# Optimization experiments

Hardware: AMD Instinct MI355X
Metric: run time of the kernel (lower is better)

The kernel has to match this reference:

```python
import jax, jax.numpy as jnp
import numpy as np

N, E, G = 30000, 480000, 64
IN, MID, HEADS, OUT = 256, (64, 64, 128), 8, 13


def _tconv(x, src, dst, ea, qw, qb, kw, kb, vw, vb, ew, sw, sb, heads, n):
    # PyG TransformerConv (concat=True, root_weight=True, beta=False), eval mode
    d = qw.shape[1] // heads
    q = (x @ qw + qb)[dst].reshape(-1, heads, d)   # [E,H,d] query at target
    k = (x @ kw + kb)[src].reshape(-1, heads, d)   # [E,H,d] key at source
    v = (x @ vw + vb)[src].reshape(-1, heads, d)   # [E,H,d] value at source
    e = (ea @ ew).reshape(-1, heads, d)            # [E,H,d] edge embedding (no bias)
    k = k + e
    a = (q * k).sum(-1) / jnp.sqrt(jnp.asarray(d, x.dtype))   # [E,H]
    amax = jax.ops.segment_max(a, dst, num_segments=n)        # segment softmax over in-edges
    ex = jnp.exp(a - amax[dst])
    den = jax.ops.segment_sum(ex, dst, num_segments=n)
    alpha = ex / den[dst]
    out = jax.ops.segment_sum((v + e) * alpha[..., None], dst, num_segments=n)
    out = out.reshape(n, heads * d)
    return out + x @ sw + sb                        # root/skip connection


def _mk(key, shape):
    return jax.random.normal(key, shape, dtype=jnp.float32) * 0.05


def setup_inputs() -> dict:
    key = jax.random.key(0)
    ks = iter(jax.random.split(key, 40))
    inp = {
        "x": jax.random.normal(next(ks), (N, IN), dtype=jnp.float32),
        "edge_index": jax.random.randint(next(ks), (2, E), 0, N, dtype=jnp.int64),
        "edge_attr": jax.random.normal(next(ks), (E, 1), dtype=jnp.float32),
        "batch": jnp.sort(jax.random.randint(next(ks), (N,), 0, G, dtype=jnp.int64)),
    }
    # conv1: in=256 -> heads=8, d=64 (out 512)
    o1 = HEADS * MID[0]
    inp.update(q1w=_mk(next(ks), (IN, o1)), q1b=_mk(next(ks), (o1,)),
               k1w=_mk(next(ks), (IN, o1)), k1b=_mk(next(ks), (o1,)),
               v1w=_mk(next(ks), (IN, o1)), v1b=_mk(next(ks), (o1,)),
               e1w=_mk(next(ks), (1, o1)),
               s1w=_mk(next(ks), (IN, o1)), s1b=_mk(next(ks), (o1,)))
    # conv2: in=512 -> heads=4, d=64 (out 256)
    h2, i2 = HEADS // 2, o1
    o2 = h2 * MID[1]
    inp.update(q2w=_mk(next(ks), (i2, o2)), q2b=_mk(next(ks), (o2,)),
               k2w=_mk(next(ks), (i2, o2)), k2b=_mk(next(ks), (o2,)),
               v2w=_mk(next(ks), (i2, o2)), v2b=_mk(next(ks), (o2,)),
               e2w=_mk(next(ks), (1, o2)),
               s2w=_mk(next(ks), (i2, o2)), s2b=_mk(next(ks), (o2,)))
    # conv3: in=256 -> heads=1, d=128
    i3, o3 = o2, MID[2]
    inp.update(q3w=_mk(next(ks), (i3, o3)), q3b=_mk(next(ks), (o3,)),
               k3w=_mk(next(ks), (i3, o3)), k3b=_mk(next(ks), (o3,)),
               v3w=_mk(next(ks), (i3, o3)), v3b=_mk(next(ks), (o3,)),
               e3w=_mk(next(ks), (1, o3)),
               s3w=_mk(next(ks), (i3, o3)), s3b=_mk(next(ks), (o3,)))
    inp.update(lw=_mk(next(ks), (MID[2], OUT)), lb=_mk(next(ks), (OUT,)))
    return inp


def reference(x, edge_index, edge_attr, batch,
              q1w, q1b, k1w, k1b, v1w, v1b, e1w, s1w, s1b,
              q2w, q2b, k2w, k2b, v2w, v2b, e2w, s2w, s2b,
              q3w, q3b, k3w, k3b, v3w, v3b, e3w, s3w, s3b,
              lw, lb):
    src, dst = edge_index[0], edge_index[1]
    h = _tconv(x, src, dst, edge_attr, q1w, q1b, k1w, k1b, v1w, v1b, e1w, s1w, s1b, HEADS, N)
    h = jax.nn.relu(h)
    h = _tconv(h, src, dst, edge_attr, q2w, q2b, k2w, k2b, v2w, v2b, e2w, s2w, s2b, HEADS // 2, N)
    h = jax.nn.relu(h)
    h = _tconv(h, src, dst, edge_attr, q3w, q3b, k3w, k3b, v3w, v3b, e3w, s3w, s3b, 1, N)
    # global mean pool over graphs
    s = jax.ops.segment_sum(h, batch, num_segments=G)
    cnt = jax.ops.segment_sum(jnp.ones((N,), h.dtype), batch, num_segments=G)
    pooled = s / jnp.maximum(cnt, 1.0)[:, None]
    return pooled @ lw + lb
```

## Files before the change

### kernel.cpp

```cpp
#include <hip/hip_runtime.h>
#include <hip/hip_bf16.h>
#include <cstdint>

#define NN 30000
#define EE 480000
#define GG 64

typedef __attribute__((ext_vector_type(8))) short bf16x8;
typedef __attribute__((ext_vector_type(4))) float float4v;
typedef __attribute__((ext_vector_type(2))) float f32x2;
typedef __attribute__((ext_vector_type(4))) unsigned short ushort4v;

static __device__ inline unsigned short f2bf(float f) {
    unsigned u = __float_as_uint(f);
    unsigned r = (u + 0x7fff + ((u >> 16) & 1)) >> 16;
    return (unsigned short)r;
}
static __device__ inline float bf2f(unsigned short u) {
    return __uint_as_float(((unsigned)u) << 16);
}

__global__ void count_deg_k(const int* __restrict__ ei, int* __restrict__ deg) {
    int e = blockIdx.x * 256 + threadIdx.x;
    if (e < EE) atomicAdd(&deg[ei[EE + e]], 1);
}

__global__ __launch_bounds__(1024) void scan_excl_k(const int* __restrict__ deg,
                                                    int* __restrict__ basep) {
    constexpr int CH = (NN + 1024) / 1024 + 1;
    __shared__ int buf[1024];
    int t = threadIdx.x;
    int b0 = t * CH;
    int loc[CH];
    int s = 0;
#pragma unroll
    for (int i = 0; i < CH; i++) {
        int idx = b0 + i;
        int v = (idx < NN) ? deg[idx] : 0;
        loc[i] = s;
        s += v;
    }
    buf[t] = s;
    __syncthreads();
    for (int off = 1; off < 1024; off <<= 1) {
        int tv = (t >= off) ? buf[t - off] : 0;
        __syncthreads();
        buf[t] += tv;
        __syncthreads();
    }
    int base = (t > 0) ? buf[t - 1] : 0;
#pragma unroll
    for (int i = 0; i < CH; i++) {
        int idx = b0 + i;
        if (idx <= NN) basep[idx] = base + loc[i];
    }
}

__global__ void fill_csr_k(const int* __restrict__ ei, const float* __restrict__ ea,
                           const int* __restrict__ basep, int* __restrict__ cnt,
                           int* __restrict__ csrc, float* __restrict__ cea) {
    int e = blockIdx.x * 256 + threadIdx.x;
    if (e < EE) {
        int d = ei[EE + e];
        int pos = basep[d] + atomicAdd(&cnt[d], 1);
        csrc[pos] = ei[e];
        cea[pos] = ea[e];
    }
}

__global__ void gbound_k(const int* __restrict__ batch, int* __restrict__ gstart) {
    int i = blockIdx.x * 256 + threadIdx.x;
    if (i >= NN) return;
    int cur = batch[i];
    if (i == 0) {
        for (int g = 0; g <= cur; ++g) gstart[g] = 0;
    } else {
        int prev = batch[i - 1];
        for (int g = prev + 1; g <= cur; ++g) gstart[g] = i;
    }
    if (i == NN - 1) {
        for (int g = cur + 1; g <= GG; ++g) gstart[g] = NN;
    }
}

struct PrepDesc { const float* src; void* dst; int rows; int cols; int blk0; int mode; };
#define NDESC 25
struct PrepArgs { PrepDesc d[NDESC]; };

__global__ __launch_bounds__(256) void prep_k(PrepArgs args) {
    int b = blockIdx.x;
    PrepDesc dd = args.d[0];
#pragma unroll
    for (int i = 1; i < NDESC; i++)
        if (b >= args.d[i].blk0) dd = args.d[i];
    int rel = b - dd.blk0;
    int total = dd.rows * dd.cols;
    int base = rel * 1024 + threadIdx.x;
    if (dd.mode == 0) {
        unsigned short* dst = (unsigned short*)dd.dst;
        for (int j = 0; j < 4; j++) {
            int i = base + j * 256;
            if (i < total) dst[i] = f2bf(dd.src[i]);
        }
    } else if (dd.mode == 1) {
        unsigned short* dst = (unsigned short*)dd.dst;
        for (int j = 0; j < 4; j++) {
            int i = base + j * 256;
            if (i < total) {
                int n = i / dd.rows, k = i - n * dd.rows;
                dst[i] = f2bf(dd.src[(size_t)k * dd.cols + n]);
            }
        }
    } else {
        float* dst = (float*)dd.dst;
        for (int j = 0; j < 4; j++) {
            int i = base + j * 256;
            if (i < total) dst[i] = dd.src[i];
        }
    }
}

__global__ __launch_bounds__(256) void pack_kv8_k(
    const unsigned short* __restrict__ QKVS, int SR, int F2,
    unsigned char* __restrict__ KV8) {
    int idx4 = blockIdx.x * 256 + threadIdx.x;
    int per_row = F2 >> 2;
    if (idx4 >= NN * per_row) return;
    int n = idx4 / per_row;
    int jj = (idx4 - n * per_row) << 2;
    const unsigned short* src = QKVS + (size_t)n * SR + (F2 >> 1) + jj;
    uint2 raw = *(const uint2*)src;
    float a = __uint_as_float(raw.x << 16);
    float b = __uint_as_float(raw.x & 0xffff0000u);
    float c = __uint_as_float(raw.y << 16);
    float d = __uint_as_float(raw.y & 0xffff0000u);
    unsigned v = 0;
    v = __builtin_amdgcn_cvt_pk_fp8_f32(a, b, v, false);
    v = __builtin_amdgcn_cvt_pk_fp8_f32(c, d, v, true);
    *(unsigned*)(KV8 + (size_t)n * F2 + jj) = v;
}

__global__ __launch_bounds__(256) void gemm_bf16_k(
    const unsigned short* __restrict__ A, const unsigned short* __restrict__ Wt,
    const float* __restrict__ bias, unsigned short* __restrict__ C,
    int M, int K, int N) {
    __shared__ unsigned short As[2][4096];
    __shared__ unsigned short Bs[2][4096];
    int tid = threadIdx.x;
    int lane = tid & 63, wid = tid >> 6;
    int wm = wid >> 1, wn = wid & 1;

    int gx = gridDim.x;
    int T = gx * gridDim.y;
    int lid = blockIdx.y * gx + blockIdx.x;
    int qq = T >> 3, rr = T & 7;
    int xcd = lid & 7, pos = lid >> 3;
    int tile = ((xcd < rr) ? xcd * (qq + 1) : rr * (qq + 1) + (xcd - rr) * qq) + pos;
    int by = tile / gx, bx = tile - by * gx;
    int row0 = by * 128, n0 = bx * 128;

    float4v acc[4][4];
#pragma unroll
    for (int i = 0; i < 4; i++)
#pragma unroll
        for (int j = 0; j < 4; j++) acc[i][j] = (float4v)0.f;

    auto stage = [&](int buf, int k0) {
#pragma unroll
        for (int i = 0; i < 2; ++i) {
            int chunkbase = i * 256 + wid * 64;
            int chunk = chunkbase + lane;
            int r = chunk & 127, kc = chunk >> 7;
            int rowA = row0 + r; if (rowA >= M) rowA = M - 1;
            const unsigned short* ga = A + (size_t)rowA * K + (k0 + kc * 8);
            __builtin_amdgcn_global_load_lds(
                (const __attribute__((address_space(1))) void*)ga,
                (__attribute__((address_space(3))) void*)(As[buf] + (size_t)chunkbase * 8),
                16, 0, 0);
            const unsigned short* gb = Wt + (size_t)(n0 + r) * K + (k0 + kc * 8);
            __builtin_amdgcn_global_load_lds(
                (const __attribute__((address_space(1))) void*)gb,
                (__attribute__((address_space(3))) void*)(Bs[buf] + (size_t)chunkbase * 8),
                16, 0, 0);
        }
    };

    stage(0, 0);
    asm volatile("s_waitcnt vmcnt(0)" ::: "memory");
    __syncthreads();

    int NT = K >> 5;
    for (int t = 0; t < NT; ++t) {
        int b = t & 1;
        if (t + 1 < NT) stage(b ^ 1, (t + 1) << 5);
        bf16x8 af[4], bfr[4];
#pragma unroll
        for (int mi = 0; mi < 4; mi++)
            af[mi] = *(const bf16x8*)(As[b] + ((lane >> 4) * 128 + wm * 64 + mi * 16 + (lane & 15)) * 8);
#pragma unroll
        for (int ni = 0; ni < 4; ni++)
            bfr[ni] = *(const bf16x8*)(Bs[b] + ((lane >> 4) * 128 + wn * 64 + ni * 16 + (lane & 15)) * 8);
#pragma unroll
        for (int mi = 0; mi < 4; mi++)
#pragma unroll
            for (int ni = 0; ni < 4; ni++)
                acc[mi][ni] = __builtin_amdgcn_mfma_f32_16x16x32_bf16(
                    bfr[ni], af[mi], acc[mi][ni], 0, 0, 0);
        asm volatile("s_waitcnt vmcnt(0)" ::: "memory");
        __syncthreads();
    }

    float4v bias4[4];
#pragma unroll
    for (int ni = 0; ni < 4; ni++)
        bias4[ni] = *(const float4v*)&bias[n0 + wn * 64 + ni * 16 + (lane >> 4) * 4];
#pragma unroll
    for (int mi = 0; mi < 4; mi++) {
        int row = row0 + wm * 64 + mi * 16 + (lane & 15);
        if (row < M) {
#pragma unroll
            for (int ni = 0; ni < 4; ni++) {
                int colb = n0 + wn * 64 + ni * 16 + (lane >> 4) * 4;
                ushort4v pk;
#pragma unroll
                for (int r = 0; r < 4; r++) pk[r] = f2bf(acc[mi][ni][r] + bias4[ni][r]);
                *(ushort4v*)(C + (size_t)row * N + colb) = pk;
            }
        }
    }
}

template <int VEC> struct RawVec;
template <> struct RawVec<2> { using T = unsigned; };
template <> struct RawVec<4> { using T = uint2; };
template <> struct RawVec<8> { using T = uint4; };

template <int VEC> struct Raw8;
template <> struct Raw8<2> { using T = unsigned short; };
template <> struct Raw8<4> { using T = unsigned; };
template <> struct Raw8<8> { using T = uint2; };

static __device__ inline void unpackr(unsigned v, float (&r)[2]) {
    r[0] = __uint_as_float(v << 16); r[1] = __uint_as_float(v & 0xffff0000u);
}
static __device__ inline void unpackr(uint2 v, float (&r)[4]) {
    r[0] = __uint_as_float(v.x << 16); r[1] = __uint_as_float(v.x & 0xffff0000u);
    r[2] = __uint_as_float(v.y << 16); r[3] = __uint_as_float(v.y & 0xffff0000u);
}
static __device__ inline void unpackr(uint4 v, float (&r)[8]) {
    r[0] = __uint_as_float(v.x << 16); r[1] = __uint_as_float(v.x & 0xffff0000u);
    r[2] = __uint_as_float(v.y << 16); r[3] = __uint_as_float(v.y & 0xffff0000u);
    r[4] = __uint_as_float(v.z << 16); r[5] = __uint_as_float(v.z & 0xffff0000u);
    r[6] = __uint_as_float(v.w << 16); r[7] = __uint_as_float(v.w & 0xffff0000u);
}

static __device__ inline void unpackf8(unsigned short v, float (&r)[2]) {
    f32x2 a = __builtin_amdgcn_cvt_pk_f32_fp8((unsigned)v, false);
    r[0] = a[0]; r[1] = a[1];
}
static __device__ inline void unpackf8(unsigned v, float (&r)[4]) {
    f32x2 a0 = __builtin_amdgcn_cvt_pk_f32_fp8(v, false);
    f32x2 a1 = __builtin_amdgcn_cvt_pk_f32_fp8(v, true);
    r[0] = a0[0]; r[1] = a0[1]; r[2] = a1[0]; r[3] = a1[1];
}
static __device__ inline void unpackf8(uint2 v, float (&r)[8]) {
    f32x2 a0 = __builtin_amdgcn_cvt_pk_f32_fp8(v.x, false);
    f32x2 a1 = __builtin_amdgcn_cvt_pk_f32_fp8(v.x, true);
    f32x2 a2 = __builtin_amdgcn_cvt_pk_f32_fp8(v.y, false);
    f32x2 a3 = __builtin_amdgcn_cvt_pk_f32_fp8(v.y, true);
    r[0] = a0[0]; r[1] = a0[1]; r[2] = a1[0]; r[3] = a1[1];
    r[4] = a2[0]; r[5] = a2[1]; r[6] = a3[0]; r[7] = a3[1];
}

template <int VEC>
__device__ inline void loadbf(const unsigned short* __restrict__ p, float (&r)[VEC]) {
    typename RawVec<VEC>::T v = *(const typename RawVec<VEC>::T*)p;
    unpackr(v, r);
}
template <int VEC>
__device__ inline void loadf32(const float* __restrict__ p, float (&r)[VEC]) {
    if constexpr (VEC == 2) {
        float2 t = *reinterpret_cast<const float2*>(p);
        r[0] = t.x; r[1] = t.y;
    } else {
#pragma unroll
        for (int i = 0; i < VEC; i += 4) {
            float4 t = *reinterpret_cast<const float4*>(p + i);
            r[i] = t.x; r[i + 1] = t.y; r[i + 2] = t.z; r[i + 3] = t.w;
        }
    }
}
template <int VEC>
__device__ inline void storebf(unsigned short* __restrict__ p, const float (&r)[VEC]) {
    unsigned w[VEC / 2];
#pragma unroll
    for (int i = 0; i < VEC / 2; i++)
        w[i] = (unsigned)f2bf(r[2 * i]) | ((unsigned)f2bf(r[2 * i + 1]) << 16);
    if constexpr (VEC == 2) *(unsigned*)p = w[0];
    else if constexpr (VEC == 4) *(uint2*)p = make_uint2(w[0], w[1]);
    else *(uint4*)p = make_uint4(w[0], w[1], w[2], w[3]);
}

template <int H, int D, bool RELU>
__global__ __launch_bounds__(256) void aggregate_k(
    const unsigned short* __restrict__ QKVS, int SR,
    const unsigned char* __restrict__ KV8,
    const float* __restrict__ ew,
    const int* __restrict__ rowptr, const int* __restrict__ csrc,
    const float* __restrict__ cea, unsigned short* __restrict__ Hout) {
    constexpr int F = H * D;
    constexpr int VEC = F / 64;
    constexpr int L = 64 / H;
    using RawT = typename Raw8<VEC>::T;
    int lane = threadIdx.x & 63;
    int node = blockIdx.x * 4 + (threadIdx.x >> 6);
    if (node >= NN) return;

    const unsigned short* qrow = QKVS + (size_t)node * SR;
    float q[VEC], ewv[VEC], acc[VEC];
    loadbf<VEC>(qrow + lane * VEC, q);
    loadf32<VEC>(ew + lane * VEC, ewv);
#pragma unroll
    for (int i = 0; i < VEC; i++) acc[i] = 0.f;

    float den = 0.f;
    const float isd = rsqrtf((float)D);
    int beg = rowptr[node], end = rowptr[node + 1];

    for (int cb = beg; cb < end; cb += 64) {
        int cnt = min(end - cb, 64);
        int gi = cb + lane;
        int sidx = (gi < end) ? csrc[gi] : 0;
        float sea = (gi < end) ? cea[gi] : 0.f;

        RawT k0r, k1r, k2r, k3r, v0r, v1r, v2r, v3r;
        float e0 = 0.f, e1 = 0.f, e2 = 0.f, e3 = 0.f;
        auto fetch = [&](int t, RawT& kr, RawT& vr, float& ea) {
            int s = __shfl(sidx, t, 64);
            ea = __shfl(sea, t, 64);
            const unsigned char* b = KV8 + (size_t)s * (2 * F) + lane * VEC;
            kr = *(const RawT*)b;
            vr = *(const RawT*)(b + F);
        };
        auto process = [&](RawT kr, RawT vr, float ea) {
            float kv[VEC], vv[VEC], t[VEC];
            unpackf8(kr, kv);
            unpackf8(vr, vv);
            float p = 0.f;
#pragma unroll
            for (int i = 0; i < VEC; i++) { t[i] = ea * ewv[i]; p += q[i] * (kv[i] + t[i]); }
#pragma unroll
            for (int off = 1; off < L; off <<= 1) p += __shfl_xor(p, off, 64);
            float w = __expf(fminf(p * isd, 30.f));
            den += w;
#pragma unroll
            for (int i = 0; i < VEC; i++) acc[i] += w * (vv[i] + t[i]);
        };

        if (cnt > 0) fetch(0, k0r, v0r, e0);
        if (cnt > 1) fetch(1, k1r, v1r, e1);
        if (cnt > 2) fetch(2, k2r, v2r, e2);
        if (cnt > 3) fetch(3, k3r, v3r, e3);

        for (int t = 0; t < cnt; t += 4) {
            process(k0r, v0r, e0);
            if (t + 4 < cnt) fetch(t + 4, k0r, v0r, e0);
            if (t + 1 < cnt) {
                process(k1r, v1r, e1);
                if (t + 5 < cnt) fetch(t + 5, k1r, v1r, e1);
            }
            if (t + 2 < cnt) {
                process(k2r, v2r, e2);
                if (t + 6 < cnt) fetch(t + 6, k2r, v2r, e2);
            }
            if (t + 3 < cnt) {
                process(k3r, v3r, e3);
                if (t + 7 < cnt) fetch(t + 7, k3r, v3r, e3);
            }
        }
    }

    float rden = (den > 0.f) ? 1.f / den : 0.f;
    float sv[VEC];
    loadbf<VEC>(qrow + 3 * F + lane * VEC, sv);
    float o[VEC];
#pragma unroll
    for (int i = 0; i < VEC; i++) {
        float v = acc[i] * rden + sv[i];
        o[i] = RELU ? fmaxf(v, 0.f) : v;
    }
    storebf<VEC>(Hout + (size_t)node * F + lane * VEC, o);
}

__global__ __launch_bounds__(256) void pool_head_k(
    const unsigned short* __restrict__ h3, const int* __restrict__ gstart,
    const float* __restrict__ lw, const float* __restrict__ lb,
    float* __restrict__ out) {
    __shared__ float part[256];
    __shared__ float pooled[128];
    int g = blockIdx.x;
    int beg = gstart[g], end = gstart[g + 1];
    int d = threadIdx.x & 127, half = threadIdx.x >> 7;
    float s = 0.f;
    for (int node = beg + half; node < end; node += 2)
        s += bf2f(h3[(size_t)node * 128 + d]);
    part[threadIdx.x] = s;
    __syncthreads();
    if (threadIdx.x < 128) {
        float cnt = fmaxf((float)(end - beg), 1.0f);
        pooled[threadIdx.x] = (part[threadIdx.x] + part[threadIdx.x + 128]) / cnt;
    }
    __syncthreads();
    if (threadIdx.x < 13) {
        float acc = lb[threadIdx.x];
        for (int dd = 0; dd < 128; ++dd)
            acc += pooled[dd] * lw[dd * 13 + threadIdx.x];
        out[g * 13 + threadIdx.x] = acc;
    }
}

__global__ void ws_fail_k(float* __restrict__ out, int n) {
    int i = blockIdx.x * 256 + threadIdx.x;
    if (i < n) out[i] = -12345.0f;
}

extern "C" void kernel_launch(void* const* d_in, const int* in_sizes, int n_in,
                              void* d_out, int out_size, void* d_ws, size_t ws_size,
                              hipStream_t stream) {
    const float* x   = (const float*)d_in[0];
    const int*   ei  = (const int*)d_in[1];
    const float* ea  = (const float*)d_in[2];
    const int*   bat = (const int*)d_in[3];
    const float* W1[4] = {(const float*)d_in[4], (const float*)d_in[6], (const float*)d_in[8], (const float*)d_in[11]};
    const float* B1[4] = {(const float*)d_in[5], (const float*)d_in[7], (const float*)d_in[9], (const float*)d_in[12]};
    const float* e1w = (const float*)d_in[10];
    const float* W2[4] = {(const float*)d_in[13], (const float*)d_in[15], (const float*)d_in[17], (const float*)d_in[20]};
    const float* B2[4] = {(const float*)d_in[14], (const float*)d_in[16], (const float*)d_in[18], (const float*)d_in[21]};
    const float* e2w = (const float*)d_in[19];
    const float* W3[4] = {(const float*)d_in[22], (const float*)d_in[24], (const float*)d_in[26], (const float*)d_in[29]};
    const float* B3[4] = {(const float*)d_in[23], (const float*)d_in[25], (const float*)d_in[27], (const float*)d_in[30]};
    const float* e3w = (const float*)d_in[28];
    const float* lw  = (const float*)d_in[31];
    const float* lb  = (const float*)d_in[32];

    char* wsb = (char*)d_ws;
    size_t off = 0;
    auto alloc_b = [&](size_t bytes) {
        void* p = wsb + off;
        off += (bytes + 255) & ~(size_t)255;
        return p;
    };
    unsigned short* xb   = (unsigned short*)alloc_b((size_t)NN * 256 * 2);
    unsigned short* Wc1  = (unsigned short*)alloc_b((size_t)2048 * 256 * 2);
    float*          bc1  = (float*)alloc_b(2048 * 4);
    unsigned short* Wc2  = (unsigned short*)alloc_b((size_t)1024 * 512 * 2);
    float*          bc2  = (float*)alloc_b(1024 * 4);
    unsigned short* Wc3  = (unsigned short*)alloc_b((size_t)512 * 256 * 2);
    float*          bc3  = (float*)alloc_b(512 * 4);
    unsigned short* QKVS = (unsigned short*)alloc_b((size_t)NN * 2048 * 2);
    unsigned char*  KV8  = (unsigned char*)alloc_b((size_t)NN * 1024);
    unsigned short* H1   = (unsigned short*)alloc_b((size_t)NN * 512 * 2);
    unsigned short* H2   = (unsigned short*)alloc_b((size_t)NN * 256 * 2);
    unsigned short* H3   = (unsigned short*)alloc_b((size_t)NN * 128 * 2);
    int*   basep  = (int*)alloc_b((NN + 1) * 4);
    int*   csrc   = (int*)alloc_b((size_t)EE * 4);
    float* cea    = (float*)alloc_b((size_t)EE * 4);
    int*   gstart = (int*)alloc_b((GG + 1) * 4);
    size_t zstart = off;
    int*   deg    = (int*)alloc_b(NN * 4);
    int*   cnt    = (int*)alloc_b(NN * 4);
    size_t zbytes = off - zstart;

    if (ws_size < off) {
        ws_fail_k<<<(out_size + 255) / 256, 256, 0, stream>>>((float*)d_out, out_size);
        return;
    }

    hipMemsetAsync(wsb + zstart, 0, zbytes, stream);

    PrepArgs pa;
    int blk = 0, di = 0;
    auto add = [&](const float* src, void* dst, int rows, int cols, int mode) {
        pa.d[di].src = src; pa.d[di].dst = dst;
        pa.d[di].rows = rows; pa.d[di].cols = cols;
        pa.d[di].mode = mode; pa.d[di].blk0 = blk;
        blk += (rows * cols + 1023) / 1024;
        di++;
    };
    add(x, xb, NN * 256, 1, 0);
    for (int s = 0; s < 4; s++) add(W1[s], Wc1 + (size_t)s * 512 * 256, 256, 512, 1);
    for (int s = 0; s < 4; s++) add(B1[s], bc1 + s * 512, 512, 1, 2);
    for (int s = 0; s < 4; s++) add(W2[s], Wc2 + (size_t)s * 256 * 512, 512, 256, 1);
    for (int s = 0; s < 4; s++) add(B2[s], bc2 + s * 256, 256, 1, 2);
    for (int s = 0; s < 4; s++) add(W3[s], Wc3 + (size_t)s * 128 * 256, 256, 128, 1);
    for (int s = 0; s < 4; s++) add(B3[s], bc3 + s * 128, 128, 1, 2);
    prep_k<<<blk, 256, 0, stream>>>(pa);

    int eblocks = (EE + 255) / 256;
    count_deg_k<<<eblocks, 256, 0, stream>>>(ei, deg);
    scan_excl_k<<<1, 1024, 0, stream>>>(deg, basep);
    fill_csr_k<<<eblocks, 256, 0, stream>>>(ei, ea, basep, cnt, csrc, cea);
    gbound_k<<<(NN + 255) / 256, 256, 0, stream>>>(bat, gstart);

    int mblocks = (NN + 127) / 128;
    auto packblocks = [](int F2) { return (NN * (F2 >> 2) + 255) / 256; };
    gemm_bf16_k<<<dim3(2048 / 128, mblocks), 256, 0, stream>>>(xb, Wc1, bc1, QKVS, NN, 256, 2048);
    pack_kv8_k<<<packblocks(1024), 256, 0, stream>>>(QKVS, 2048, 1024, KV8);
    aggregate_k<8, 64, true><<<NN / 4, 256, 0, stream>>>(QKVS, 2048, KV8, e1w, basep, csrc, cea, H1);
    gemm_bf16_k<<<dim3(1024 / 128, mblocks), 256, 0, stream>>>(H1, Wc2, bc2, QKVS, NN, 512, 1024);
    pack_kv8_k<<<packblocks(512), 256, 0, stream>>>(QKVS, 1024, 512, KV8);
    aggregate_k<4, 64, true><<<NN / 4, 256, 0, stream>>>(QKVS, 1024, KV8, e2w, basep, csrc, cea, H2);
    gemm_bf16_k<<<dim3(512 / 128, mblocks), 256, 0, stream>>>(H2, Wc3, bc3, QKVS, NN, 256, 512);
    pack_kv8_k<<<packblocks(256), 256, 0, stream>>>(QKVS, 512, 256, KV8);
    aggregate_k<1, 128, false><<<NN / 4, 256, 0, stream>>>(QKVS, 512, KV8, e3w, basep, csrc, cea, H3);

    pool_head_k<<<GG, 256, 0, stream>>>(H3, gstart, lw, lb, (float*)d_out);
}
```

Baseline: 723.1 us.

## Fuse FP8 K/V packing into GEMM epilogue and triple-buffer GEMM loads

The separate pack_kv8_k kernel is removed. The GEMM epilogue now writes the FP8 copy of the K/V columns straight from the fp32 accumulators, which saves three launches and a full re-read of the bf16 K/V slice per layer. The GEMM mainloop also moves from two to three LDS buffers with a partial vmcnt wait, so loads are issued two tiles ahead. FP8 values are now converted from fp32 rather than from rounded bf16, which may change results slightly, and LDS use per block grows.

Result: no change. 728.8 us (+0.8%).

```diff
diff --git a/kernel.cpp b/kernel.cpp
--- a/kernel.cpp
+++ b/kernel.cpp
@@ -120,32 +120,13 @@
     }
 }
 
-__global__ __launch_bounds__(256) void pack_kv8_k(
-    const unsigned short* __restrict__ QKVS, int SR, int F2,
-    unsigned char* __restrict__ KV8) {
-    int idx4 = blockIdx.x * 256 + threadIdx.x;
-    int per_row = F2 >> 2;
-    if (idx4 >= NN * per_row) return;
-    int n = idx4 / per_row;
-    int jj = (idx4 - n * per_row) << 2;
-    const unsigned short* src = QKVS + (size_t)n * SR + (F2 >> 1) + jj;
-    uint2 raw = *(const uint2*)src;
-    float a = __uint_as_float(raw.x << 16);
-    float b = __uint_as_float(raw.x & 0xffff0000u);
-    float c = __uint_as_float(raw.y << 16);
-    float d = __uint_as_float(raw.y & 0xffff0000u);
-    unsigned v = 0;
-    v = __builtin_amdgcn_cvt_pk_fp8_f32(a, b, v, false);
-    v = __builtin_amdgcn_cvt_pk_fp8_f32(c, d, v, true);
-    *(unsigned*)(KV8 + (size_t)n * F2 + jj) = v;
-}
-
 __global__ __launch_bounds__(256) void gemm_bf16_k(
     const unsigned short* __restrict__ A, const unsigned short* __restrict__ Wt,
     const float* __restrict__ bias, unsigned short* __restrict__ C,
+    unsigned char* __restrict__ KV8,
     int M, int K, int N) {
-    __shared__ unsigned short As[2][4096];
-    __shared__ unsigned short Bs[2][4096];
+    __shared__ unsigned short As[3][4096];
+    __shared__ unsigned short Bs[3][4096];
     int tid = threadIdx.x;
     int lane = tid & 63, wid = tid >> 6;
     int wm = wid >> 1, wn = wid & 1;
@@ -165,7 +146,8 @@
 #pragma unroll
         for (int j = 0; j < 4; j++) acc[i][j] = (float4v)0.f;
 
-    auto stage = [&](int buf, int k0) {
+    auto stage = [&](int buf, int t) {
+        int k0 = t << 5;
 #pragma unroll
         for (int i = 0; i < 2; ++i) {
             int chunkbase = i * 256 + wid * 64;
@@ -185,14 +167,17 @@
         }
     };
 
+    int NT = K >> 5;
     stage(0, 0);
-    asm volatile("s_waitcnt vmcnt(0)" ::: "memory");
-    __syncthreads();
-
-    int NT = K >> 5;
+    stage(1, 1);
+
     for (int t = 0; t < NT; ++t) {
-        int b = t & 1;
-        if (t + 1 < NT) stage(b ^ 1, (t + 1) << 5);
+        int b = t % 3;
+        if (t + 1 < NT) asm volatile("s_waitcnt vmcnt(4)" ::: "memory");
+        else            asm volatile("s_waitcnt vmcnt(0)" ::: "memory");
+        __syncthreads();
+        if (t + 2 < NT) stage((t + 2) % 3, t + 2);
+
         bf16x8 af[4], bfr[4];
 #pragma unroll
         for (int mi = 0; mi < 4; mi++)
@@ -206,10 +191,9 @@
             for (int ni = 0; ni < 4; ni++)
                 acc[mi][ni] = __builtin_amdgcn_mfma_f32_16x16x32_bf16(
                     bfr[ni], af[mi], acc[mi][ni], 0, 0, 0);
-        asm volatile("s_waitcnt vmcnt(0)" ::: "memory");
-        __syncthreads();
-    }
-
+    }
+
+    int kvlo = N >> 2, kvhi = 3 * (N >> 2);
     float4v bias4[4];
 #pragma unroll
     for (int ni = 0; ni < 4; ni++)
@@ -221,10 +205,19 @@
 #pragma unroll
             for (int ni = 0; ni < 4; ni++) {
                 int colb = n0 + wn * 64 + ni * 16 + (lane >> 4) * 4;
+                float v0 = acc[mi][ni][0] + bias4[ni][0];
+                float v1 = acc[mi][ni][1] + bias4[ni][1];
+                float v2 = acc[mi][ni][2] + bias4[ni][2];
+                float v3 = acc[mi][ni][3] + bias4[ni][3];
                 ushort4v pk;
-#pragma unroll
-                for (int r = 0; r < 4; r++) pk[r] = f2bf(acc[mi][ni][r] + bias4[ni][r]);
+                pk[0] = f2bf(v0); pk[1] = f2bf(v1); pk[2] = f2bf(v2); pk[3] = f2bf(v3);
                 *(ushort4v*)(C + (size_t)row * N + colb) = pk;
+                if (colb >= kvlo && colb < kvhi) {
+                    unsigned q = 0;
+                    q = __builtin_amdgcn_cvt_pk_fp8_f32(v0, v1, q, false);
+                    q = __builtin_amdgcn_cvt_pk_fp8_f32(v2, v3, q, true);
+                    *(unsigned*)(KV8 + (size_t)row * (N >> 1) + (colb - kvlo)) = q;
+                }
             }
         }
     }
@@ -503,15 +496,11 @@
     gbound_k<<<(NN + 255) / 256, 256, 0, stream>>>(bat, gstart);
 
     int mblocks = (NN + 127) / 128;
-    auto packblocks = [](int F2) { return (NN * (F2 >> 2) + 255) / 256; };
-    gemm_bf16_k<<<dim3(2048 / 128, mblocks), 256, 0, stream>>>(xb, Wc1, bc1, QKVS, NN, 256, 2048);
-    pack_kv8_k<<<packblocks(1024), 256, 0, stream>>>(QKVS, 2048, 1024, KV8);
+    gemm_bf16_k<<<dim3(2048 / 128, mblocks), 256, 0, stream>>>(xb, Wc1, bc1, QKVS, KV8, NN, 256, 2048);
     aggregate_k<8, 64, true><<<NN / 4, 256, 0, stream>>>(QKVS, 2048, KV8, e1w, basep, csrc, cea, H1);
-    gemm_bf16_k<<<dim3(1024 / 128, mblocks), 256, 0, stream>>>(H1, Wc2, bc2, QKVS, NN, 512, 1024);
-    pack_kv8_k<<<packblocks(512), 256, 0, stream>>>(QKVS, 1024, 512, KV8);
+    gemm_bf16_k<<<dim3(1024 / 128, mblocks), 256, 0, stream>>>(H1, Wc2, bc2, QKVS, KV8, NN, 512, 1024);
     aggregate_k<4, 64, true><<<NN / 4, 256, 0, stream>>>(QKVS, 1024, KV8, e2w, basep, csrc, cea, H2);
-    gemm_bf16_k<<<dim3(512 / 128, mblocks), 256, 0, stream>>>(H2, Wc3, bc3, QKVS, NN, 256, 512);
-    pack_kv8_k<<<packblocks(256), 256, 0, stream>>>(QKVS, 512, 256, KV8);
+    gemm_bf16_k<<<dim3(512 / 128, mblocks), 256, 0, stream>>>(H2, Wc3, bc3, QKVS, KV8, NN, 256, 512);
     aggregate_k<1, 128, false><<<NN / 4, 256, 0, stream>>>(QKVS, 512, KV8, e3w, basep, csrc, cea, H3);
 
     pool_head_k<<<GG, 256, 0, stream>>>(H3, gstart, lw, lb, (float*)d_out);
```
